# Optimization experiments

Measured on AMD Instinct MI355X. Metric: run time of the kernel, lower is better.

Reference implementation:

```python
import jax, jax.numpy as jnp
import numpy as np

B, S, D, HD, NH = 1, 2048, 1024, 64, 16
INV_SQRT = 1.0 / HD ** 0.5


def _rope_tables(seq_len, head_dim):
    inv_freq = 1.0 / 10000.0 ** (np.arange(0, head_dim, 2, dtype=np.float32) / head_dim)
    t = np.arange(seq_len, dtype=np.float32)
    freqs = t[:, None] * inv_freq[None, :]            # [S, HD/2]
    emb = np.concatenate([freqs, freqs], axis=1)      # [S, HD]
    cos = jnp.asarray(np.cos(emb), dtype=jnp.float32)[None, :, :, None]  # [1,S,HD,1]
    sin = jnp.asarray(np.sin(emb), dtype=jnp.float32)[None, :, :, None]
    return cos, sin

COS, SIN = _rope_tables(S, HD)


def _rotate_half(x):
    # NB: faithful to original torch code: chunk on LAST axis, which is the HEADS axis here
    x1, x2 = jnp.split(x, 2, axis=-1)
    return jnp.concatenate([-x2, x1], axis=-1)


def setup_inputs() -> dict:
    key = jax.random.key(0)
    ks = jax.random.split(key, 8)
    x = jax.random.normal(ks[0], (B, S, D), dtype=jnp.float32)
    bias = jax.random.normal(ks[1], (B, S, S, NH), dtype=jnp.float32)
    mask = jax.random.randint(ks[2], (B, S, S, NH), 0, 2, dtype=jnp.int32)
    w_qkv = jax.random.normal(ks[3], (3 * NH * HD, D), dtype=jnp.float32) * 0.02
    b_qkv = jnp.zeros((3 * NH * HD,), dtype=jnp.float32)
    w_out = jax.random.normal(ks[4], (D, NH * HD), dtype=jnp.float32) * 0.02
    b_out = jnp.zeros((D,), dtype=jnp.float32)
    return {"x": x, "bias": bias, "mask": mask, "w_qkv": w_qkv, "b_qkv": b_qkv,
            "w_out": w_out, "b_out": b_out}


def reference(x, bias, mask, w_qkv, b_qkv, w_out, b_out):
    qkv = x @ w_qkv.T + b_qkv                         # [B,S,3*NH*HD]
    q, k, v = jnp.split(qkv, 3, axis=-1)
    # torch .view((..., head_dim, n_heads)): last dim splits row-major into (HD, NH)
    q = q.reshape(B, S, HD, NH)
    k = k.reshape(B, S, HD, NH)
    v = v.reshape(B, S, HD, NH)
    # inline RoPE (rotate_half over the heads axis, as in the original code)
    cos = COS[:, :S]
    sin = SIN[:, :S]
    q = q * cos + _rotate_half(q) * sin
    k = k * cos + _rotate_half(k) * sin
    attn_score = INV_SQRT * jnp.einsum('bjdh,bkdh->bjkh', q, k)  # [B,S,S,NH]
    attn_score = attn_score + bias
    attn_score = jnp.where(mask == 0, jnp.float32(-1e8), attn_score)
    attn_logits = jax.nn.softmax(attn_score, axis=2)
    attn = jnp.einsum('bjkh,bkdh->bjdh', attn_logits, v)          # [B,S,HD,NH]
    out = attn.reshape(B, S, HD * NH) @ w_out.T + b_out           # [B,S,D]
    return out
```

## Files before the change

### kernel.cpp

```cpp
#include <hip/hip_runtime.h>
#include <stdint.h>
#include <math.h>

using f32x4  = __attribute__((ext_vector_type(4)))  float;
using f32x16 = __attribute__((ext_vector_type(16))) float;
using s16x8  = __attribute__((ext_vector_type(8)))  short;

#define DI __device__ __forceinline__

DI unsigned short f2bf(float f) {
  unsigned u = __float_as_uint(f);
  u += 0x7FFFu + ((u >> 16) & 1u);
  return (unsigned short)(u >> 16);
}
DI float bf2f(unsigned short h) { return __uint_as_float((unsigned)h << 16); }

__global__ void k_cvt_bf16(const float* __restrict__ in, unsigned short* __restrict__ out, int n4) {
  int i = blockIdx.x * blockDim.x + threadIdx.x;
  const int stride = gridDim.x * blockDim.x;
  for (; i < n4; i += stride) {
    float4 v = reinterpret_cast<const float4*>(in)[i];
    ushort4 o;
    o.x = f2bf(v.x); o.y = f2bf(v.y); o.z = f2bf(v.z); o.w = f2bf(v.w);
    reinterpret_cast<ushort4*>(out)[i] = o;
  }
}

__global__ void k_rope_table(float* __restrict__ cost, float* __restrict__ sint) {
  const int idx = blockIdx.x * 256 + threadIdx.x;
  const int s = idx >> 5, fi = idx & 31;
  const double invf = pow(10000.0, -(double)fi / 32.0);
  const float ang = (float)s * (float)invf;
  cost[idx] = (float)cos((double)ang);
  sint[idx] = (float)sin((double)ang);
}

__global__ __launch_bounds__(256) void k_gemm_bt(
    const unsigned short* __restrict__ A, const unsigned short* __restrict__ B,
    const float* __restrict__ bias, float* __restrict__ C, int M, int N, int K) {
  __shared__ unsigned short As[128 * 32], Bs[128 * 32];
  const int tid = threadIdx.x, l = tid & 63, w = tid >> 6;
  const int wr = w >> 1, wc = w & 1;
  const int m0 = blockIdx.x * 128, n0 = blockIdx.y * 128;
  const int srow = tid >> 2, scol = (tid & 3) * 8;
  f32x4 acc[4][4] = {};
  for (int k0 = 0; k0 < K; k0 += 32) {
    s16x8 a0 = *(const s16x8*)(A + (size_t)(m0 + srow) * K + k0 + scol);
    s16x8 a1 = *(const s16x8*)(A + (size_t)(m0 + 64 + srow) * K + k0 + scol);
    s16x8 b0 = *(const s16x8*)(B + (size_t)(n0 + srow) * K + k0 + scol);
    s16x8 b1 = *(const s16x8*)(B + (size_t)(n0 + 64 + srow) * K + k0 + scol);
    __syncthreads();
    *(s16x8*)&As[srow * 32 + scol] = a0;
    *(s16x8*)&As[(64 + srow) * 32 + scol] = a1;
    *(s16x8*)&Bs[srow * 32 + scol] = b0;
    *(s16x8*)&Bs[(64 + srow) * 32 + scol] = b1;
    __syncthreads();
    s16x8 af[4], bf[4];
#pragma unroll
    for (int i = 0; i < 4; i++)
      af[i] = *(const s16x8*)&As[(wr * 64 + i * 16 + (l & 15)) * 32 + (l >> 4) * 8];
#pragma unroll
    for (int j = 0; j < 4; j++)
      bf[j] = *(const s16x8*)&Bs[(wc * 64 + j * 16 + (l & 15)) * 32 + (l >> 4) * 8];
#pragma unroll
    for (int i = 0; i < 4; i++)
#pragma unroll
      for (int j = 0; j < 4; j++)
        acc[i][j] = __builtin_amdgcn_mfma_f32_16x16x32_bf16(af[i], bf[j], acc[i][j], 0, 0, 0);
  }
#pragma unroll
  for (int i = 0; i < 4; i++) {
    const int row = m0 + wr * 64 + i * 16 + (l >> 4) * 4;
#pragma unroll
    for (int j = 0; j < 4; j++) {
      const int col = n0 + wc * 64 + j * 16 + (l & 15);
      const float bv = bias ? bias[col] : 0.f;
#pragma unroll
      for (int r = 0; r < 4; r++) C[(size_t)(row + r) * N + col] = acc[i][j][r] + bv;
    }
  }
}

__global__ void k_rope_relayout(const float* __restrict__ qkv, const float* __restrict__ cost,
                                const float* __restrict__ sint,
                                unsigned short* __restrict__ qh, unsigned short* __restrict__ kh,
                                unsigned short* __restrict__ vt) {
  const int s = blockIdx.x, t = threadIdx.x;
  const float* row = qkv + (size_t)s * 3072;
  const int c = t * 4;
  const int d = c >> 4;
  const int hbase = c & 15;
  const float cv = cost[s * 32 + (d & 31)];
  const float sv = sint[s * 32 + (d & 31)];
  const float sgn = (hbase < 8) ? -1.f : 1.f;
  {
    float4 v = *(const float4*)(row + c);
    float4 v2 = *(const float4*)(row + (c ^ 8));
    const float* vp = (const float*)&v;
    const float* vp2 = (const float*)&v2;
#pragma unroll
    for (int i = 0; i < 4; i++) {
      float val = vp[i] * cv + sgn * vp2[i] * sv;
      qh[(size_t)(hbase + i) * (2048 * 64) + s * 64 + d] = f2bf(val);
    }
  }
  {
    float4 v = *(const float4*)(row + 1024 + c);
    float4 v2 = *(const float4*)(row + 1024 + (c ^ 8));
    const float* vp = (const float*)&v;
    const float* vp2 = (const float*)&v2;
#pragma unroll
    for (int i = 0; i < 4; i++) {
      float val = vp[i] * cv + sgn * vp2[i] * sv;
      kh[(size_t)(hbase + i) * (2048 * 64) + s * 64 + d] = f2bf(val);
    }
  }
  {
    float4 v = *(const float4*)(row + 2048 + c);
    const float* vp = (const float*)&v;
#pragma unroll
    for (int i = 0; i < 4; i++)
      vt[(size_t)(hbase + i) * (64 * 2048) + (size_t)d * 2048 + s] = f2bf(vp[i]);
  }
}

__global__ void k_mask(const float* __restrict__ bias, const int* __restrict__ mask,
                       unsigned short* __restrict__ bm16, int n8) {
  int i = blockIdx.x * blockDim.x + threadIdx.x;
  const int stride = gridDim.x * blockDim.x;
  for (; i < n8; i += stride) {
    float4 b0 = reinterpret_cast<const float4*>(bias)[2 * i];
    float4 b1 = reinterpret_cast<const float4*>(bias)[2 * i + 1];
    int4 m0 = reinterpret_cast<const int4*>(mask)[2 * i];
    int4 m1 = reinterpret_cast<const int4*>(mask)[2 * i + 1];
    uint4 o;
    o.x = (unsigned)f2bf(m0.x ? b0.x : -1.0e8f) | ((unsigned)f2bf(m0.y ? b0.y : -1.0e8f) << 16);
    o.y = (unsigned)f2bf(m0.z ? b0.z : -1.0e8f) | ((unsigned)f2bf(m0.w ? b0.w : -1.0e8f) << 16);
    o.z = (unsigned)f2bf(m1.x ? b1.x : -1.0e8f) | ((unsigned)f2bf(m1.y ? b1.y : -1.0e8f) << 16);
    o.w = (unsigned)f2bf(m1.z ? b1.z : -1.0e8f) | ((unsigned)f2bf(m1.w ? b1.w : -1.0e8f) << 16);
    reinterpret_cast<uint4*>(bm16)[i] = o;
  }
}

#define GLDS16(gp, lp)                                                            \
  __builtin_amdgcn_global_load_lds(                                               \
      (const __attribute__((address_space(1))) unsigned int*)(const void*)(gp),   \
      (__attribute__((address_space(3))) unsigned int*)(void*)(lp), 16, 0, 0)

__global__ __launch_bounds__(1024) void k_attn(
    const unsigned short* __restrict__ bm16,
    const unsigned short* __restrict__ qh, const unsigned short* __restrict__ kh,
    const unsigned short* __restrict__ vt,
    float* __restrict__ Opart, float* __restrict__ ML) {
  __shared__ unsigned short tile[3][32][512];
  const int tid = threadIdx.x, l = tid & 63, w = tid >> 6;
  const int hi = l >> 5, ln = l & 31;
  const int jt = blockIdx.x, ks = blockIdx.y;
  const int j0 = jt * 32, kstart = ks * 512;

  s16x8 qf[4];
  {
    const unsigned short* qb = qh + ((size_t)w * 2048 + (j0 + ln)) * 64 + 8 * hi;
#pragma unroll
    for (int ds = 0; ds < 4; ds++) qf[ds] = *(const s16x8*)(qb + ds * 16);
  }
  const unsigned short* kb = kh + ((size_t)w * 2048 + (kstart + ln)) * 64 + 8 * hi;
  const unsigned short* vb = vt + (size_t)w * 64 * 2048 + (size_t)ln * 2048 + kstart + 8 * hi;

  const int jr0 = 2 * w, jr1 = 2 * w + 1;
  const unsigned short* src0 = bm16 + ((size_t)(j0 + jr0) << 15) + (size_t)kstart * 16 + ((l ^ jr0) << 3);
  const unsigned short* src1 = bm16 + ((size_t)(j0 + jr1) << 15) + (size_t)kstart * 16 + ((l ^ jr1) << 3);

#define STAGE(m)                                           \
  {                                                        \
    const int bi_ = (m) % 3;                               \
    GLDS16(src0 + (size_t)(m) * 512, &tile[bi_][jr0][0]);  \
    GLDS16(src1 + (size_t)(m) * 512, &tile[bi_][jr1][0]);  \
  }

  f32x16 o0 = {}, o1 = {};
  float mrun = -3.0e38f, lrun = 0.f;

  STAGE(0)

  for (int m = 0; m < 16; ++m) {
    if (m + 1 < 16) {
      STAGE(m + 1)
      asm volatile("s_waitcnt vmcnt(2)\n\ts_barrier" ::: "memory");
    } else {
      asm volatile("s_waitcnt vmcnt(0)\n\ts_barrier" ::: "memory");
    }
    const int bi = m % 3;
    s16x8 kf[4], vf[4];
    {
      const unsigned short* kp = kb + (size_t)m * (32 * 64);
#pragma unroll
      for (int ds = 0; ds < 4; ds++) kf[ds] = *(const s16x8*)(kp + ds * 16);
      const unsigned short* vp = vb + (size_t)m * 32;
      vf[0] = *(const s16x8*)(vp);
      vf[1] = *(const s16x8*)(vp + 32 * 2048);
      vf[2] = *(const s16x8*)(vp + 16);
      vf[3] = *(const s16x8*)(vp + 32 * 2048 + 16);
    }
    f32x16 st = {};
#pragma unroll
    for (int ds = 0; ds < 4; ds++)
      st = __builtin_amdgcn_mfma_f32_32x32x16_bf16(kf[ds], qf[ds], st, 0, 0, 0);
    float p[16];
    float tmax = -3.0e38f;
#pragma unroll
    for (int r = 0; r < 16; r++) {
      const int kl = (r & 3) + 8 * (r >> 2) + 4 * hi;
      const int slot = kl * 2 + (w >> 3);
      const unsigned short u = tile[bi][ln][((slot ^ ln) << 3) + (w & 7)];
      const float sv = st[r] * 0.125f + bf2f(u);
      p[r] = sv;
      tmax = fmaxf(tmax, sv);
    }
    tmax = fmaxf(tmax, __shfl_xor(tmax, 32));
    const float mnew = fmaxf(mrun, tmax);
    const float sc = __expf(mrun - mnew);
    float psum = 0.f;
#pragma unroll
    for (int r = 0; r < 16; r++) { p[r] = __expf(p[r] - mnew); psum += p[r]; }
    psum += __shfl_xor(psum, 32);
    lrun = lrun * sc + psum;
    mrun = mnew;
#pragma unroll
    for (int r = 0; r < 16; r++) {
      const int jj = (r & 3) + 8 * (r >> 2) + 4 * hi;
      const float s2 = __shfl(sc, jj);
      o0[r] *= s2;
      o1[r] *= s2;
    }
    unsigned pk[8];
#pragma unroll
    for (int q = 0; q < 8; q++)
      pk[q] = (unsigned)f2bf(p[2 * q]) | ((unsigned)f2bf(p[2 * q + 1]) << 16);
#pragma unroll
    for (int s = 0; s < 2; s++) {
      const unsigned a0 = pk[4 * s + 0], a1 = pk[4 * s + 1];
      const unsigned a2 = pk[4 * s + 2], a3 = pk[4 * s + 3];
      const unsigned x0 = (unsigned)__shfl_xor((int)a0, 32);
      const unsigned x1 = (unsigned)__shfl_xor((int)a1, 32);
      const unsigned x2 = (unsigned)__shfl_xor((int)a2, 32);
      const unsigned x3 = (unsigned)__shfl_xor((int)a3, 32);
      union { int4 i; s16x8 v; } u;
      u.i.x = (int)(hi ? x2 : a0);
      u.i.y = (int)(hi ? x3 : a1);
      u.i.z = (int)(hi ? a2 : x0);
      u.i.w = (int)(hi ? a3 : x1);
      o0 = __builtin_amdgcn_mfma_f32_32x32x16_bf16(u.v, vf[2 * s + 0], o0, 0, 0, 0);
      o1 = __builtin_amdgcn_mfma_f32_32x32x16_bf16(u.v, vf[2 * s + 1], o1, 0, 0, 0);
    }
  }
#undef STAGE

  float* ob = Opart + (((size_t)(ks * 64 + jt) * 16 + w) * 32) * 64;
#pragma unroll
  for (int r = 0; r < 16; r++) {
    const int jj = (r & 3) + 8 * (r >> 2) + 4 * hi;
    ob[(size_t)jj * 64 + ln] = o0[r];
    ob[(size_t)jj * 64 + 32 + ln] = o1[r];
  }
  if (hi == 0) {
    float* mlp = ML + (((size_t)(ks * 64 + jt) * 16 + w) * 32 + ln) * 2;
    mlp[0] = mrun;
    mlp[1] = lrun;
  }
}

__global__ void k_combine(const float* __restrict__ Opart, const float* __restrict__ ML,
                          unsigned short* __restrict__ attn_flat) {
  const int j = blockIdx.x, t = threadIdx.x;
  const int jt = j >> 5, jl = j & 31;
  const int d = t >> 2;
  unsigned short tmp[4];
#pragma unroll
  for (int q = 0; q < 4; q++) {
    const int hh = 4 * (t & 3) + q;
    float m[4], lv[4];
#pragma unroll
    for (int ksi = 0; ksi < 4; ksi++) {
      const size_t base = ((size_t)(ksi * 64 + jt) * 16 + hh) * 32 + jl;
      m[ksi] = ML[base * 2];
      lv[ksi] = ML[base * 2 + 1];
    }
    const float M = fmaxf(fmaxf(m[0], m[1]), fmaxf(m[2], m[3]));
    float L = 0.f, acc = 0.f;
#pragma unroll
    for (int ksi = 0; ksi < 4; ksi++) {
      const float e = __expf(m[ksi] - M);
      L += lv[ksi] * e;
      const size_t base = ((size_t)(ksi * 64 + jt) * 16 + hh) * 32 + jl;
      acc += Opart[base * 64 + d] * e;
    }
    tmp[q] = f2bf(acc / L);
  }
  ushort4 outv;
  outv.x = tmp[0]; outv.y = tmp[1]; outv.z = tmp[2]; outv.w = tmp[3];
  *(ushort4*)(attn_flat + (size_t)j * 1024 + t * 4) = outv;
}

extern "C" void kernel_launch(void* const* d_in, const int* in_sizes, int n_in,
                              void* d_out, int out_size, void* d_ws, size_t ws_size,
                              hipStream_t stream) {
  const float* x     = (const float*)d_in[0];
  const float* bias  = (const float*)d_in[1];
  const int*   mask  = (const int*)d_in[2];
  const float* w_qkv = (const float*)d_in[3];
  const float* b_qkv = (const float*)d_in[4];
  const float* w_out = (const float*)d_in[5];
  const float* b_out = (const float*)d_in[6];
  float* out = (float*)d_out;

  char* ws = (char*)d_ws;
  unsigned short* xb   = (unsigned short*)(ws);
  unsigned short* wqb  = (unsigned short*)(ws + ((size_t)4 << 20));
  unsigned short* wob  = (unsigned short*)(ws + ((size_t)10 << 20));
  float* cost          = (float*)(ws + ((size_t)12 << 20));
  float* sint          = (float*)(ws + ((size_t)12 << 20) + (256 << 10));
  float* qkv           = (float*)(ws + ((size_t)13 << 20));
  unsigned short* qhp  = (unsigned short*)(ws + ((size_t)37 << 20));
  unsigned short* khp  = (unsigned short*)(ws + ((size_t)41 << 20));
  unsigned short* vtp  = (unsigned short*)(ws + ((size_t)45 << 20));
  unsigned short* af   = (unsigned short*)(ws + ((size_t)49 << 20));
  float* Opart         = (float*)(ws + ((size_t)53 << 20));
  float* ML            = (float*)(ws + ((size_t)88 << 20));
  unsigned short* bm16 = (unsigned short*)(ws + ((size_t)90 << 20));

  k_cvt_bf16<<<dim3(512), dim3(256), 0, stream>>>(x, xb, 2048 * 1024 / 4);
  k_cvt_bf16<<<dim3(512), dim3(256), 0, stream>>>(w_qkv, wqb, 3072 * 1024 / 4);
  k_cvt_bf16<<<dim3(512), dim3(256), 0, stream>>>(w_out, wob, 1024 * 1024 / 4);
  k_rope_table<<<dim3(256), dim3(256), 0, stream>>>(cost, sint);
  k_mask<<<dim3(2048), dim3(256), 0, stream>>>(bias, mask, bm16, 2048 * 2048 * 16 / 8);
  k_gemm_bt<<<dim3(16, 24), dim3(256), 0, stream>>>(xb, wqb, b_qkv, qkv, 2048, 3072, 1024);
  k_rope_relayout<<<dim3(2048), dim3(256), 0, stream>>>(qkv, cost, sint, qhp, khp, vtp);
  k_attn<<<dim3(64, 4), dim3(1024), 0, stream>>>(bm16, qhp, khp, vtp, Opart, ML);
  k_combine<<<dim3(2048), dim3(256), 0, stream>>>(Opart, ML, af);
  k_gemm_bt<<<dim3(16, 8), dim3(256), 0, stream>>>(af, wob, b_out, out, 2048, 1024, 1024);
}
```

Baseline: 352.5 us.

## Split attention blocks across head groups and issue K/V loads before barrier

The attention kernel now launches 512-thread blocks covering 8 heads each, with head groups as a new grid dimension. This doubles the block count and is meant to raise occupancy and improve load balance. The bias/mask LDS tile is re-laid out per head group with a new XOR swizzle, and K/V fragment loads are hoisted above the stage-wait barrier so they overlap the next bias tile's async copy. The mask-conversion kernel also processes 16 elements per thread instead of 8. The costs are that each block now reads only 8 of the 16 heads' bias bytes per row, giving shorter contiguous segments, and the new swizzle must stay correct.

```diff
diff --git a/kernel.cpp b/kernel.cpp
--- a/kernel.cpp
+++ b/kernel.cpp
@@ -125,20 +125,29 @@
 }
 
 __global__ void k_mask(const float* __restrict__ bias, const int* __restrict__ mask,
-                       unsigned short* __restrict__ bm16, int n8) {
+                       unsigned short* __restrict__ bm16, int n16) {
   int i = blockIdx.x * blockDim.x + threadIdx.x;
   const int stride = gridDim.x * blockDim.x;
-  for (; i < n8; i += stride) {
-    float4 b0 = reinterpret_cast<const float4*>(bias)[2 * i];
-    float4 b1 = reinterpret_cast<const float4*>(bias)[2 * i + 1];
-    int4 m0 = reinterpret_cast<const int4*>(mask)[2 * i];
-    int4 m1 = reinterpret_cast<const int4*>(mask)[2 * i + 1];
-    uint4 o;
-    o.x = (unsigned)f2bf(m0.x ? b0.x : -1.0e8f) | ((unsigned)f2bf(m0.y ? b0.y : -1.0e8f) << 16);
-    o.y = (unsigned)f2bf(m0.z ? b0.z : -1.0e8f) | ((unsigned)f2bf(m0.w ? b0.w : -1.0e8f) << 16);
-    o.z = (unsigned)f2bf(m1.x ? b1.x : -1.0e8f) | ((unsigned)f2bf(m1.y ? b1.y : -1.0e8f) << 16);
-    o.w = (unsigned)f2bf(m1.z ? b1.z : -1.0e8f) | ((unsigned)f2bf(m1.w ? b1.w : -1.0e8f) << 16);
-    reinterpret_cast<uint4*>(bm16)[i] = o;
+  for (; i < n16; i += stride) {
+    float4 b0 = reinterpret_cast<const float4*>(bias)[4 * i];
+    float4 b1 = reinterpret_cast<const float4*>(bias)[4 * i + 1];
+    float4 b2 = reinterpret_cast<const float4*>(bias)[4 * i + 2];
+    float4 b3 = reinterpret_cast<const float4*>(bias)[4 * i + 3];
+    int4 m0 = reinterpret_cast<const int4*>(mask)[4 * i];
+    int4 m1 = reinterpret_cast<const int4*>(mask)[4 * i + 1];
+    int4 m2 = reinterpret_cast<const int4*>(mask)[4 * i + 2];
+    int4 m3 = reinterpret_cast<const int4*>(mask)[4 * i + 3];
+    uint4 o0, o1;
+    o0.x = (unsigned)f2bf(m0.x ? b0.x : -1.0e8f) | ((unsigned)f2bf(m0.y ? b0.y : -1.0e8f) << 16);
+    o0.y = (unsigned)f2bf(m0.z ? b0.z : -1.0e8f) | ((unsigned)f2bf(m0.w ? b0.w : -1.0e8f) << 16);
+    o0.z = (unsigned)f2bf(m1.x ? b1.x : -1.0e8f) | ((unsigned)f2bf(m1.y ? b1.y : -1.0e8f) << 16);
+    o0.w = (unsigned)f2bf(m1.z ? b1.z : -1.0e8f) | ((unsigned)f2bf(m1.w ? b1.w : -1.0e8f) << 16);
+    o1.x = (unsigned)f2bf(m2.x ? b2.x : -1.0e8f) | ((unsigned)f2bf(m2.y ? b2.y : -1.0e8f) << 16);
+    o1.y = (unsigned)f2bf(m2.z ? b2.z : -1.0e8f) | ((unsigned)f2bf(m2.w ? b2.w : -1.0e8f) << 16);
+    o1.z = (unsigned)f2bf(m3.x ? b3.x : -1.0e8f) | ((unsigned)f2bf(m3.y ? b3.y : -1.0e8f) << 16);
+    o1.w = (unsigned)f2bf(m3.z ? b3.z : -1.0e8f) | ((unsigned)f2bf(m3.w ? b3.w : -1.0e8f) << 16);
+    reinterpret_cast<uint4*>(bm16)[2 * i] = o0;
+    reinterpret_cast<uint4*>(bm16)[2 * i + 1] = o1;
   }
 }
 
@@ -147,35 +156,36 @@
       (const __attribute__((address_space(1))) unsigned int*)(const void*)(gp),   \
       (__attribute__((address_space(3))) unsigned int*)(void*)(lp), 16, 0, 0)
 
-__global__ __launch_bounds__(1024) void k_attn(
+__global__ __launch_bounds__(512, 4) void k_attn(
     const unsigned short* __restrict__ bm16,
     const unsigned short* __restrict__ qh, const unsigned short* __restrict__ kh,
     const unsigned short* __restrict__ vt,
     float* __restrict__ Opart, float* __restrict__ ML) {
-  __shared__ unsigned short tile[3][32][512];
+  __shared__ unsigned short tile[3][32][32][8];
   const int tid = threadIdx.x, l = tid & 63, w = tid >> 6;
   const int hi = l >> 5, ln = l & 31;
-  const int jt = blockIdx.x, ks = blockIdx.y;
-  const int j0 = jt * 32, kstart = ks * 512;
+  const int hg = blockIdx.x, jt = blockIdx.y, ks = blockIdx.z;
+  const int j0 = jt * 32, kstart = ks * 512, h = hg * 8 + w;
 
   s16x8 qf[4];
   {
-    const unsigned short* qb = qh + ((size_t)w * 2048 + (j0 + ln)) * 64 + 8 * hi;
+    const unsigned short* qb = qh + ((size_t)h * 2048 + (j0 + ln)) * 64 + 8 * hi;
 #pragma unroll
     for (int ds = 0; ds < 4; ds++) qf[ds] = *(const s16x8*)(qb + ds * 16);
   }
-  const unsigned short* kb = kh + ((size_t)w * 2048 + (kstart + ln)) * 64 + 8 * hi;
-  const unsigned short* vb = vt + (size_t)w * 64 * 2048 + (size_t)ln * 2048 + kstart + 8 * hi;
-
-  const int jr0 = 2 * w, jr1 = 2 * w + 1;
-  const unsigned short* src0 = bm16 + ((size_t)(j0 + jr0) << 15) + (size_t)kstart * 16 + ((l ^ jr0) << 3);
-  const unsigned short* src1 = bm16 + ((size_t)(j0 + jr1) << 15) + (size_t)kstart * 16 + ((l ^ jr1) << 3);
-
-#define STAGE(m)                                           \
-  {                                                        \
-    const int bi_ = (m) % 3;                               \
-    GLDS16(src0 + (size_t)(m) * 512, &tile[bi_][jr0][0]);  \
-    GLDS16(src1 + (size_t)(m) * 512, &tile[bi_][jr1][0]);  \
+  const unsigned short* kb = kh + ((size_t)h * 2048 + (kstart + ln)) * 64 + 8 * hi;
+  const unsigned short* vb = vt + (size_t)h * 64 * 2048 + (size_t)ln * 2048 + kstart + 8 * hi;
+
+  const int jr0 = 4 * w + hi;
+  const int jr1 = jr0 + 2;
+  const unsigned short* src0 = bm16 + ((size_t)(j0 + jr0) * 2048 + kstart + (ln ^ (jr0 & 7))) * 16 + hg * 8;
+  const unsigned short* src1 = bm16 + ((size_t)(j0 + jr1) * 2048 + kstart + (ln ^ (jr1 & 7))) * 16 + hg * 8;
+
+#define STAGE(m)                                            \
+  {                                                         \
+    const int bi_ = (m) % 3;                                \
+    GLDS16(src0 + (size_t)(m) * 512, &tile[bi_][4 * w][0][0]);      \
+    GLDS16(src1 + (size_t)(m) * 512, &tile[bi_][4 * w + 2][0][0]);  \
   }
 
   f32x16 o0 = {}, o1 = {};
@@ -184,13 +194,6 @@
   STAGE(0)
 
   for (int m = 0; m < 16; ++m) {
-    if (m + 1 < 16) {
-      STAGE(m + 1)
-      asm volatile("s_waitcnt vmcnt(2)\n\ts_barrier" ::: "memory");
-    } else {
-      asm volatile("s_waitcnt vmcnt(0)\n\ts_barrier" ::: "memory");
-    }
-    const int bi = m % 3;
     s16x8 kf[4], vf[4];
     {
       const unsigned short* kp = kb + (size_t)m * (32 * 64);
@@ -202,6 +205,13 @@
       vf[2] = *(const s16x8*)(vp + 16);
       vf[3] = *(const s16x8*)(vp + 32 * 2048 + 16);
     }
+    if (m + 1 < 16) {
+      STAGE(m + 1)
+      asm volatile("s_waitcnt vmcnt(2)\n\ts_barrier" ::: "memory");
+    } else {
+      asm volatile("s_waitcnt vmcnt(0)\n\ts_barrier" ::: "memory");
+    }
+    const int bi = m % 3;
     f32x16 st = {};
 #pragma unroll
     for (int ds = 0; ds < 4; ds++)
@@ -211,8 +221,7 @@
 #pragma unroll
     for (int r = 0; r < 16; r++) {
       const int kl = (r & 3) + 8 * (r >> 2) + 4 * hi;
-      const int slot = kl * 2 + (w >> 3);
-      const unsigned short u = tile[bi][ln][((slot ^ ln) << 3) + (w & 7)];
+      const unsigned short u = tile[bi][ln][kl ^ (ln & 7)][w];
       const float sv = st[r] * 0.125f + bf2f(u);
       p[r] = sv;
       tmax = fmaxf(tmax, sv);
@@ -256,7 +265,7 @@
   }
 #undef STAGE
 
-  float* ob = Opart + (((size_t)(ks * 64 + jt) * 16 + w) * 32) * 64;
+  float* ob = Opart + (((size_t)(ks * 64 + jt) * 16 + h) * 32) * 64;
 #pragma unroll
   for (int r = 0; r < 16; r++) {
     const int jj = (r & 3) + 8 * (r >> 2) + 4 * hi;
@@ -264,7 +273,7 @@
     ob[(size_t)jj * 64 + 32 + ln] = o1[r];
   }
   if (hi == 0) {
-    float* mlp = ML + (((size_t)(ks * 64 + jt) * 16 + w) * 32 + ln) * 2;
+    float* mlp = ML + (((size_t)(ks * 64 + jt) * 16 + h) * 32 + ln) * 2;
     mlp[0] = mrun;
     mlp[1] = lrun;
   }
@@ -333,10 +342,10 @@
   k_cvt_bf16<<<dim3(512), dim3(256), 0, stream>>>(w_qkv, wqb, 3072 * 1024 / 4);
   k_cvt_bf16<<<dim3(512), dim3(256), 0, stream>>>(w_out, wob, 1024 * 1024 / 4);
   k_rope_table<<<dim3(256), dim3(256), 0, stream>>>(cost, sint);
-  k_mask<<<dim3(2048), dim3(256), 0, stream>>>(bias, mask, bm16, 2048 * 2048 * 16 / 8);
+  k_mask<<<dim3(2048), dim3(256), 0, stream>>>(bias, mask, bm16, 2048 * 2048 * 16 / 16);
   k_gemm_bt<<<dim3(16, 24), dim3(256), 0, stream>>>(xb, wqb, b_qkv, qkv, 2048, 3072, 1024);
   k_rope_relayout<<<dim3(2048), dim3(256), 0, stream>>>(qkv, cost, sint, qhp, khp, vtp);
-  k_attn<<<dim3(64, 4), dim3(1024), 0, stream>>>(bm16, qhp, khp, vtp, Opart, ML);
+  k_attn<<<dim3(2, 64, 4), dim3(512), 0, stream>>>(bm16, qhp, khp, vtp, Opart, ML);
   k_combine<<<dim3(2048), dim3(256), 0, stream>>>(Opart, ML, af);
   k_gemm_bt<<<dim3(16, 8), dim3(256), 0, stream>>>(af, wob, b_out, out, 2048, 1024, 1024);
 }
```

New measurement: 400.8 us. 13.7% more time.
